# Optimization experiments

Hardware: AMD Instinct MI355X
Metric: run time of the kernel (lower is better)

## Reference

```python
import jax, jax.numpy as jnp
import numpy as np

D_MODEL = 1024
N_HEADS = 16
D_K = 64
D_FF = 4096
B = 8
S = 1024
NEG = -1e32
EPS = 1e-5


def _layer_norm(x, g, b):
    mu = jnp.mean(x, axis=-1, keepdims=True)
    var = jnp.var(x, axis=-1, keepdims=True)
    return (x - mu) * jax.lax.rsqrt(var + EPS) * g + b


def setup_inputs() -> dict:
    key = jax.random.key(0)
    ks = jax.random.split(key, 16)
    sc = 0.02
    inp = {
        'x': jax.random.normal(ks[0], (B, S, D_MODEL), dtype=jnp.float32),
        'Wq': jax.random.normal(ks[1], (D_MODEL, D_MODEL), jnp.float32) * sc,
        'bq': jnp.zeros((D_MODEL,), jnp.float32),
        'Wk': jax.random.normal(ks[2], (D_MODEL, D_MODEL), jnp.float32) * sc,
        'bk': jnp.zeros((D_MODEL,), jnp.float32),
        'Wv': jax.random.normal(ks[3], (D_MODEL, D_MODEL), jnp.float32) * sc,
        'bv': jnp.zeros((D_MODEL,), jnp.float32),
        'Wo': jax.random.normal(ks[4], (D_MODEL, D_MODEL), jnp.float32) * sc,
        'bo': jnp.zeros((D_MODEL,), jnp.float32),
        'W1': jax.random.normal(ks[5], (D_MODEL, D_FF), jnp.float32) * sc,
        'b1': jnp.zeros((D_FF,), jnp.float32),
        'W2': jax.random.normal(ks[6], (D_FF, D_MODEL), jnp.float32) * sc,
        'b2': jnp.zeros((D_MODEL,), jnp.float32),
        'g1': jnp.ones((D_MODEL,), jnp.float32),
        'beta1': jnp.zeros((D_MODEL,), jnp.float32),
        'g3': jnp.ones((D_MODEL,), jnp.float32),
        'beta3': jnp.zeros((D_MODEL,), jnp.float32),
    }
    return inp


def _block(x, Wq, bq, Wk, bk, Wv, bv, Wo, bo, W1, b1, W2, b2, g1, beta1, g3, beta3):
    bs, seqlen, _ = x.shape
    # QKV projections -> [b, h, s, d_k]
    def split_heads(t):
        return t.reshape(bs, seqlen, N_HEADS, D_K).transpose(0, 2, 1, 3)
    q = split_heads(x @ Wq + bq)
    k = split_heads(x @ Wk + bk)
    v = split_heads(x @ Wv + bv)
    # scores [b,h,s,s]
    scores = jnp.einsum('bhqd,bhkd->bhqk', q, k) / jnp.sqrt(jnp.float32(D_K))
    # mask=0 case: src_mask = (triu(ones, k=0) == 0) -> allow strictly lower (j < i)
    i = jnp.arange(seqlen)[:, None]
    j = jnp.arange(seqlen)[None, :]
    allowed = (j < i)  # [s, s]
    scores = jnp.where(allowed[None, None], scores, NEG)
    attn = jax.nn.softmax(scores, axis=-1)
    # zero_pad: zero out the first query row of attention probs
    attn = attn * (i > 0).astype(attn.dtype)[None, None]
    ctx = jnp.einsum('bhqk,bhkd->bhqd', attn, v)  # [b,h,s,d_k]
    concat = ctx.transpose(0, 2, 1, 3).reshape(bs, seqlen, D_MODEL)
    attn_out = concat @ Wo + bo
    # residual + LN (dropout p=0)
    h1 = _layer_norm(x + attn_out, g1, beta1)
    # position-wise FFN
    ffn = jax.nn.relu(h1 @ W1 + b1) @ W2 + b2
    out = _layer_norm(h1 + ffn, g3, beta3)
    return out


def reference(x, Wq, bq, Wk, bk, Wv, bv, Wo, bo, W1, b1, W2, b2, g1, beta1, g3, beta3):
    return _block(x, Wq, bq, Wk, bk, Wv, bv, Wo, bo, W1, b1, W2, b2, g1, beta1, g3, beta3)
```

## Files before the change

### kernel.cpp

```cpp
#include <hip/hip_runtime.h>
#include <hip/hip_bf16.h>

typedef __bf16 bf16x8 __attribute__((ext_vector_type(8)));
typedef __bf16 bf16x4 __attribute__((ext_vector_type(4)));
typedef float f32x4 __attribute__((ext_vector_type(4)));
typedef float f32x16 __attribute__((ext_vector_type(16)));

#define GLOBAL_LOAD_LDS16(gp, lp)                                              \
  __builtin_amdgcn_global_load_lds(                                            \
      (const __attribute__((address_space(1))) void*)(gp),                     \
      (__attribute__((address_space(3))) void*)(lp), 16, 0, 0)

__global__ __launch_bounds__(256) void transpose4_f2b_k(
    const float* __restrict__ s0, const float* __restrict__ s1,
    const float* __restrict__ s2, const float* __restrict__ s3,
    __bf16* __restrict__ dst) {
  __shared__ float tile[32][33];
  const float* srcs[4] = {s0, s1, s2, s3};
  const float* src = srcs[blockIdx.z];
  __bf16* d = dst + ((size_t)blockIdx.z << 20);
  const int bx = blockIdx.x * 32, by = blockIdx.y * 32;
  const int tx = threadIdx.x & 31, ty = threadIdx.x >> 5;
#pragma unroll
  for (int i = 0; i < 32; i += 8)
    tile[ty + i][tx] = src[(size_t)(by + ty + i) * 1024 + bx + tx];
  __syncthreads();
#pragma unroll
  for (int i = 0; i < 32; i += 8)
    d[(size_t)(bx + ty + i) * 1024 + by + tx] = (__bf16)tile[tx][ty + i];
}

__global__ __launch_bounds__(256) void transpose_f2b_k(
    const float* __restrict__ src, __bf16* __restrict__ dst, int R, int C) {
  __shared__ float tile[32][33];
  const int bx = blockIdx.x * 32, by = blockIdx.y * 32;
  const int tx = threadIdx.x & 31, ty = threadIdx.x >> 5;
#pragma unroll
  for (int i = 0; i < 32; i += 8)
    tile[ty + i][tx] = src[(size_t)(by + ty + i) * C + bx + tx];
  __syncthreads();
#pragma unroll
  for (int i = 0; i < 32; i += 8)
    dst[(size_t)(bx + ty + i) * R + by + tx] = (__bf16)tile[tx][ty + i];
}

__global__ __launch_bounds__(256) void transpose_v_k(
    const __bf16* __restrict__ src, __bf16* __restrict__ dst) {
  __shared__ __bf16 tile[32][33];
  const int bh = blockIdx.z;
  const int s0 = blockIdx.x * 32, d0 = blockIdx.y * 32;
  const size_t base = (size_t)bh << 16;
  const int tx = threadIdx.x & 31, ty = threadIdx.x >> 5;
#pragma unroll
  for (int i = 0; i < 32; i += 8)
    tile[ty + i][tx] = src[base + (size_t)(s0 + ty + i) * 64 + d0 + tx];
  __syncthreads();
#pragma unroll
  for (int i = 0; i < 32; i += 8)
    dst[base + (size_t)(d0 + ty + i) * 1024 + s0 + tx] = tile[tx][ty + i];
}

__global__ __launch_bounds__(256) void convert_f2b_k(const float* __restrict__ s,
                                                     __bf16* __restrict__ d) {
  const size_t i = ((size_t)blockIdx.x * 256 + threadIdx.x) * 4;
  const float4 v = *(const float4*)(s + i);
  bf16x4 o;
  o[0] = (__bf16)v.x; o[1] = (__bf16)v.y; o[2] = (__bf16)v.z; o[3] = (__bf16)v.w;
  *(bf16x4*)(d + i) = o;
}

__global__ void concat3_k(const float* a, const float* b, const float* c,
                          float* o) {
  int i = blockIdx.x * 256 + threadIdx.x;
  if (i < 1024) o[i] = a[i];
  else if (i < 2048) o[i] = b[i - 1024];
  else if (i < 3072) o[i] = c[i - 2048];
}

#define STG(P, rowbase, Kld, kbase, DST)                                       \
  do {                                                                         \
    GLOBAL_LOAD_LDS16((P) + (size_t)((rowbase) + wave * 16 + srow) * (Kld) +   \
                          (kbase) + sch8,                                      \
                      (DST) + wave * 1024);                                    \
    GLOBAL_LOAD_LDS16((P) + (size_t)((rowbase) + wave * 16 + 8 + srow) *       \
                              (Kld) + (kbase) + sch8,                          \
                      (DST) + wave * 1024 + 512);                              \
  } while (0)

#define LDA(BUF, HALF)                                                         \
  do {                                                                         \
    const __bf16* pA_ = &As[BUF][HALF][aoff];                                  \
    _Pragma("unroll") for (int f_ = 0; f_ < 4; ++f_) {                         \
      af[f_][0] = *(const bf16x8*)(pA_ + f_ * 1024 + c0);                      \
      af[f_][1] = *(const bf16x8*)(pA_ + f_ * 1024 + (c0 ^ 32));               \
    }                                                                          \
  } while (0)

#define LDB(BUF, CB)                                                           \
  do {                                                                         \
    const __bf16* pB_ = &Bs[BUF][CB][boff];                                    \
    _Pragma("unroll") for (int g_ = 0; g_ < 2; ++g_) {                         \
      bfr[CB][g_][0] = *(const bf16x8*)(pB_ + g_ * 1024 + c0);                 \
      bfr[CB][g_][1] = *(const bf16x8*)(pB_ + g_ * 1024 + (c0 ^ 32));          \
    }                                                                          \
  } while (0)

#define MFMA16(rb, cb)                                                         \
  do {                                                                         \
    _Pragma("unroll") for (int f_ = 0; f_ < 4; ++f_)                           \
        _Pragma("unroll") for (int g_ = 0; g_ < 2; ++g_) {                     \
      acc[rb][f_][cb][g_] = __builtin_amdgcn_mfma_f32_16x16x32_bf16(           \
          af[f_][0], bfr[cb][g_][0], acc[rb][f_][cb][g_], 0, 0, 0);            \
      acc[rb][f_][cb][g_] = __builtin_amdgcn_mfma_f32_16x16x32_bf16(           \
          af[f_][1], bfr[cb][g_][1], acc[rb][f_][cb][g_], 0, 0, 0);            \
    }                                                                          \
  } while (0)

#define PH_MID()                                                               \
  do {                                                                         \
    asm volatile("" ::: "memory");                                             \
    __builtin_amdgcn_s_barrier();                                              \
    asm volatile("s_waitcnt lgkmcnt(0)" ::: "memory");                         \
    __builtin_amdgcn_s_setprio(1);                                             \
  } while (0)

#define PH_END()                                                               \
  do {                                                                         \
    __builtin_amdgcn_s_setprio(0);                                             \
    asm volatile("" ::: "memory");                                             \
    __builtin_amdgcn_s_barrier();                                              \
    asm volatile("" ::: "memory");                                             \
  } while (0)

#define PH_END_VM(NVM)                                                         \
  do {                                                                         \
    __builtin_amdgcn_s_setprio(0);                                             \
    asm volatile("s_waitcnt vmcnt(" #NVM ")" ::: "memory");                    \
    __builtin_amdgcn_s_barrier();                                              \
    asm volatile("" ::: "memory");                                             \
  } while (0)

template <int EPI>
__global__ __launch_bounds__(512, 2) void gemm256(const __bf16* __restrict__ A,
                                                  const __bf16* __restrict__ Bt,
                                                  const float* __restrict__ bias,
                                                  __bf16* __restrict__ C,
                                                  int M, int N, int K) {
  __shared__ __align__(16) __bf16 As[2][2][128 * 64];
  __shared__ __align__(16) __bf16 Bs[2][2][128 * 64];
  const int tid = threadIdx.x;
  const int wave = tid >> 6, lane = tid & 63;
  const int quad = lane >> 4, l15 = lane & 15;
  const int wm = wave >> 2, wn = wave & 3;

  const int nwg = gridDim.x;
  const int cpx = nwg >> 3;
  const int bid = blockIdx.x;
  const int wg = (bid & 7) * cpx + (bid >> 3);
  const int gy = N >> 8;
  const int tm = wg / gy, tn = wg - tm * gy;
  const int m0 = tm << 8, n0 = tn << 8;

  const int srow = lane >> 3;
  const int sch8 = ((lane & 7) ^ srow) * 8;
  const int aoff = (wm * 64 + l15) * 64;
  const int boff = (wn * 32 + l15) * 64;
  const int c0 = (quad ^ (l15 & 7)) * 8;

  bf16x8 af[4][2], bfr[2][2][2];
  f32x4 acc[2][4][2][2] = {};

  const int NJ = K >> 7;

  STG(A, m0, K, 0, &As[0][0][0]);
  STG(Bt, n0, K, 0, &Bs[0][0][0]);
  STG(A, m0 + 128, K, 0, &As[0][1][0]);
  STG(Bt, n0 + 128, K, 0, &Bs[0][1][0]);
  STG(A, m0, K, 64, &As[1][0][0]);
  STG(Bt, n0, K, 64, &Bs[1][0][0]);
  asm volatile("s_waitcnt vmcnt(4)" ::: "memory");
  __builtin_amdgcn_s_barrier();
  asm volatile("" ::: "memory");

  for (int j = 0; j < NJ; ++j) {
    const int t1k = (j << 7) + 64, t2k = (j << 7) + 128, t3k = (j << 7) + 192;
    const bool pf = (j + 1 < NJ);
    LDA(0, 0);
    LDB(0, 0);
    STG(A, m0 + 128, K, t1k, &As[1][1][0]);
    PH_MID();
    MFMA16(0, 0);
    PH_END();
    LDB(0, 1);
    STG(Bt, n0 + 128, K, t1k, &Bs[1][1][0]);
    PH_MID();
    MFMA16(0, 1);
    PH_END();
    LDA(0, 1);
    if (pf) STG(A, m0, K, t2k, &As[0][0][0]);
    PH_MID();
    MFMA16(1, 0);
    PH_END();
    if (pf) STG(Bt, n0, K, t2k, &Bs[0][0][0]);
    PH_MID();
    MFMA16(1, 1);
    if (pf) PH_END_VM(4); else PH_END_VM(0);
    LDA(1, 0);
    LDB(1, 0);
    if (pf) STG(A, m0 + 128, K, t2k, &As[0][1][0]);
    PH_MID();
    MFMA16(0, 0);
    PH_END();
    LDB(1, 1);
    if (pf) STG(Bt, n0 + 128, K, t2k, &Bs[0][1][0]);
    PH_MID();
    MFMA16(0, 1);
    PH_END();
    LDA(1, 1);
    if (pf) STG(A, m0, K, t3k, &As[1][0][0]);
    PH_MID();
    MFMA16(1, 0);
    PH_END();
    if (pf) STG(Bt, n0, K, t3k, &Bs[1][0][0]);
    PH_MID();
    MFMA16(1, 1);
    if (pf) PH_END_VM(4); else PH_END();
  }

  float bvv[2][2];
#pragma unroll
  for (int cb = 0; cb < 2; ++cb)
#pragma unroll
    for (int g = 0; g < 2; ++g)
      bvv[cb][g] = bias[n0 + cb * 128 + wn * 32 + g * 16 + l15];
#pragma unroll
  for (int rb = 0; rb < 2; ++rb)
#pragma unroll
    for (int f = 0; f < 4; ++f)
#pragma unroll
      for (int i = 0; i < 4; ++i) {
        const int row = m0 + rb * 128 + wm * 64 + f * 16 + quad * 4 + i;
#pragma unroll
        for (int cb = 0; cb < 2; ++cb)
#pragma unroll
          for (int g = 0; g < 2; ++g) {
            const int col = n0 + cb * 128 + wn * 32 + g * 16 + l15;
            float v = acc[rb][f][cb][g][i] + bvv[cb][g];
            if (EPI == 1) v = fmaxf(v, 0.0f);
            size_t oidx;
            if (EPI == 2) {
              const int which = col >> 10, wi = col & 1023;
              const int h = wi >> 6, d = wi & 63;
              const int b = row >> 10, s = row & 1023;
              oidx = ((size_t)which << 23) +
                     (((size_t)(b * 16 + h) << 16) + s * 64 + d);
            } else {
              oidx = (size_t)row * N + col;
            }
            C[oidx] = (__bf16)v;
          }
      }
}

__global__ __launch_bounds__(256) void gemm_bt64(const __bf16* __restrict__ A,
                                                 const __bf16* __restrict__ Bt,
                                                 const float* __restrict__ bias,
                                                 __bf16* __restrict__ C,
                                                 int M, int N, int K) {
  __shared__ __align__(16) __bf16 As[128 * 64];
  __shared__ __align__(16) __bf16 Bs[64 * 64];
  const int tid = threadIdx.x;
  const int wave = tid >> 6, lane = tid & 63;
  const int quad = lane >> 4, l15 = lane & 15;
  const int wm = wave >> 1, wn = wave & 1;
  const int m0 = blockIdx.x * 128, n0 = blockIdx.y * 64;
  const int srow = tid >> 3;
  const int sch = tid & 7;

  f32x4 acc[4][2] = {};

  for (int k0 = 0; k0 < K; k0 += 64) {
#pragma unroll
    for (int p = 0; p < 4; ++p) {
      const int row = p * 32 + srow;
      GLOBAL_LOAD_LDS16(A + (size_t)(m0 + row) * K + k0 + ((sch ^ (row & 7)) * 8),
                        As + p * 2048 + wave * 512);
    }
#pragma unroll
    for (int p = 0; p < 2; ++p) {
      const int row = p * 32 + srow;
      GLOBAL_LOAD_LDS16(Bt + (size_t)(n0 + row) * K + k0 + ((sch ^ (row & 7)) * 8),
                        Bs + p * 2048 + wave * 512);
    }
    __syncthreads();
    bf16x8 af[4][2], bfr[2][2];
#pragma unroll
    for (int kk = 0; kk < 2; ++kk) {
#pragma unroll
      for (int mt = 0; mt < 4; ++mt) {
        const int row = wm * 64 + mt * 16 + l15;
        af[mt][kk] =
            *(const bf16x8*)(As + row * 64 + (((kk * 4 + quad) ^ (row & 7)) * 8));
      }
#pragma unroll
      for (int nt = 0; nt < 2; ++nt) {
        const int row = wn * 32 + nt * 16 + l15;
        bfr[nt][kk] =
            *(const bf16x8*)(Bs + row * 64 + (((kk * 4 + quad) ^ (row & 7)) * 8));
      }
    }
#pragma unroll
    for (int kk = 0; kk < 2; ++kk)
#pragma unroll
      for (int mt = 0; mt < 4; ++mt)
#pragma unroll
        for (int nt = 0; nt < 2; ++nt)
          acc[mt][nt] = __builtin_amdgcn_mfma_f32_16x16x32_bf16(
              af[mt][kk], bfr[nt][kk], acc[mt][nt], 0, 0, 0);
    __syncthreads();
  }

  float bv[2];
#pragma unroll
  for (int nt = 0; nt < 2; ++nt) bv[nt] = bias[n0 + wn * 32 + nt * 16 + l15];
#pragma unroll
  for (int mt = 0; mt < 4; ++mt) {
#pragma unroll
    for (int r = 0; r < 4; ++r) {
      const int row = m0 + wm * 64 + mt * 16 + quad * 4 + r;
#pragma unroll
      for (int nt = 0; nt < 2; ++nt) {
        const int col = n0 + wn * 32 + nt * 16 + l15;
        C[(size_t)row * N + col] = (__bf16)(acc[mt][nt][r] + bv[nt]);
      }
    }
  }
}

__global__ __launch_bounds__(256) void attn_kernel(const __bf16* __restrict__ Q,
                                                   const __bf16* __restrict__ Kg,
                                                   const __bf16* __restrict__ Vt,
                                                   __bf16* __restrict__ ctx) {
  const int qp = blockIdx.x;
  const int bh = blockIdx.y;
  const int b = bh >> 4, h = bh & 15;
  const int tid = threadIdx.x, wave = tid >> 6, lane = tid & 63;
  const int quad = lane >> 4, l15 = lane & 15;
  const size_t hoff = (size_t)bh << 16;
  const __bf16* Qh = Q + hoff;
  const __bf16* Kh = Kg + hoff;
  const __bf16* Vh = Vt + hoff;

  __shared__ __align__(16) __bf16 Ks[64 * 64];
  __shared__ __align__(16) __bf16 Vs[64 * 64];
  __shared__ __align__(16) __bf16 Ps[4][32 * 72];
  __shared__ float lL[128];

  const int skey = wave * 8 + (lane >> 3);
  const int sgr = lane & 7;

#pragma unroll
  for (int pass = 0; pass < 2; ++pass) {
    const int qt = pass ? (7 - qp) : qp;
    const int qb = qt * 128;

    bf16x8 qf[2][2];
#pragma unroll
    for (int g = 0; g < 2; ++g) {
      const int qrow = qb + wave * 32 + g * 16 + l15;
      bf16x8 t0 = *(const bf16x8*)(Qh + (size_t)qrow * 64 + quad * 8);
      bf16x8 t1 = *(const bf16x8*)(Qh + (size_t)qrow * 64 + 32 + quad * 8);
#pragma unroll
      for (int e = 0; e < 8; ++e) {
        qf[g][0][e] = (__bf16)((float)t0[e] * 0.125f);
        qf[g][1][e] = (__bf16)((float)t1[e] * 0.125f);
      }
    }

    f32x4 oacc[4][2] = {};
    float lrun[2][4] = {};

    const int ktmax = 2 * qt + 1;
    for (int kt = 0; kt <= ktmax; ++kt) {
      __syncthreads();
#pragma unroll
      for (int j = 0; j < 2; ++j) {
        const int row = skey + 32 * j;
        GLOBAL_LOAD_LDS16(
            Kh + (size_t)(kt * 64 + row) * 64 + ((sgr ^ (row & 7)) * 8),
            Ks + j * 2048 + wave * 512);
        GLOBAL_LOAD_LDS16(
            Vh + (size_t)row * 1024 + kt * 64 + ((sgr ^ (row & 7)) * 8),
            Vs + j * 2048 + wave * 512);
      }
      __syncthreads();

      f32x4 sacc[2][4] = {};
#pragma unroll
      for (int nt = 0; nt < 4; ++nt) {
        const int key = nt * 16 + l15, sw = key & 7;
        bf16x8 kf0 = *(const bf16x8*)(Ks + key * 64 + ((quad ^ sw) * 8));
        bf16x8 kf1 = *(const bf16x8*)(Ks + key * 64 + (((quad + 4) ^ sw) * 8));
#pragma unroll
        for (int g = 0; g < 2; ++g) {
          sacc[g][nt] = __builtin_amdgcn_mfma_f32_16x16x32_bf16(
              qf[g][0], kf0, sacc[g][nt], 0, 0, 0);
          sacc[g][nt] = __builtin_amdgcn_mfma_f32_16x16x32_bf16(
              qf[g][1], kf1, sacc[g][nt], 0, 0, 0);
        }
      }

      const bool tilemask = (kt >= 2 * qt);
#pragma unroll
      for (int g = 0; g < 2; ++g)
#pragma unroll
        for (int nt = 0; nt < 4; ++nt) {
          const int key = kt * 64 + nt * 16 + l15;
#pragma unroll
          for (int r = 0; r < 4; ++r) {
            float p = __expf(fminf(sacc[g][nt][r], 60.0f));
            if (tilemask && key >= qb + wave * 32 + g * 16 + quad * 4 + r)
              p = 0.0f;
            sacc[g][nt][r] = p;
            lrun[g][r] += p;
          }
        }

#pragma unroll
      for (int g = 0; g < 2; ++g)
#pragma unroll
        for (int nt = 0; nt < 4; ++nt)
#pragma unroll
          for (int r = 0; r < 4; ++r)
            Ps[wave][(g * 16 + quad * 4 + r) * 72 + nt * 16 + l15] =
                (__bf16)sacc[g][nt][r];

#pragma unroll
      for (int kc = 0; kc < 2; ++kc) {
        bf16x8 pf[2];
#pragma unroll
        for (int g = 0; g < 2; ++g)
          pf[g] = *(const bf16x8*)(&Ps[wave][(g * 16 + l15) * 72 + kc * 32 +
                                             quad * 8]);
#pragma unroll
        for (int mdt = 0; mdt < 4; ++mdt) {
          const int d = mdt * 16 + l15, sw = d & 7;
          bf16x8 vf =
              *(const bf16x8*)(Vs + d * 64 + (((kc * 4 + quad) ^ sw) * 8));
#pragma unroll
          for (int g = 0; g < 2; ++g)
            oacc[mdt][g] = __builtin_amdgcn_mfma_f32_16x16x32_bf16(
                vf, pf[g], oacc[mdt][g], 0, 0, 0);
        }
      }
    }

#pragma unroll
    for (int g = 0; g < 2; ++g)
#pragma unroll
      for (int r = 0; r < 4; ++r) {
        float s = lrun[g][r];
#pragma unroll
        for (int d = 1; d < 16; d <<= 1) s += __shfl_xor(s, d);
        if (l15 == 0) lL[wave * 32 + g * 16 + quad * 4 + r] = s;
      }
    float linv[2];
#pragma unroll
    for (int g = 0; g < 2; ++g) {
      const float l = lL[wave * 32 + g * 16 + l15];
      linv[g] = (qb + wave * 32 + g * 16 + l15 == 0) ? 0.0f : (1.0f / l);
    }
    __bf16* Ot = Ps[wave];
#pragma unroll
    for (int mdt = 0; mdt < 4; ++mdt)
#pragma unroll
      for (int g = 0; g < 2; ++g)
#pragma unroll
        for (int r = 0; r < 4; ++r)
          Ot[(g * 16 + l15) * 72 + mdt * 16 + quad * 4 + r] =
              (__bf16)(oacc[mdt][g][r] * linv[g]);
#pragma unroll
    for (int rr = 0; rr < 2; ++rr)
#pragma unroll
      for (int j = 0; j < 2; ++j) {
        const int row = rr * 16 + (lane >> 2), chk = (lane & 3) + 4 * j;
        bf16x8 ov = *(const bf16x8*)(Ot + row * 72 + chk * 8);
        const size_t oi = ((size_t)(b * 1024 + qb + wave * 32 + row)) * 1024 +
                          h * 64 + chk * 8;
        *(bf16x8*)(ctx + oi) = ov;
      }
  }
}

template <typename TX, typename TY, typename TO>
__global__ __launch_bounds__(256) void add_ln_kernel(const TX* __restrict__ x,
                                                     const TY* __restrict__ y,
                                                     const float* __restrict__ g,
                                                     const float* __restrict__ be,
                                                     TO* __restrict__ out) {
  const int row = blockIdx.x;
  const size_t base = (size_t)row * 1024;
  const int t = threadIdx.x;
  float xv[4], yv[4];
  if constexpr (sizeof(TX) == 4) {
    const float4 a = *(const float4*)(x + base + t * 4);
    xv[0] = a.x; xv[1] = a.y; xv[2] = a.z; xv[3] = a.w;
  } else {
    const bf16x4 a = *(const bf16x4*)(x + base + t * 4);
#pragma unroll
    for (int i = 0; i < 4; ++i) xv[i] = (float)a[i];
  }
  if constexpr (sizeof(TY) == 4) {
    const float4 a = *(const float4*)(y + base + t * 4);
    yv[0] = a.x; yv[1] = a.y; yv[2] = a.z; yv[3] = a.w;
  } else {
    const bf16x4 a = *(const bf16x4*)(y + base + t * 4);
#pragma unroll
    for (int i = 0; i < 4; ++i) yv[i] = (float)a[i];
  }
  float v[4], s = 0.0f, s2 = 0.0f;
#pragma unroll
  for (int i = 0; i < 4; ++i) {
    v[i] = xv[i] + yv[i];
    s += v[i];
    s2 += v[i] * v[i];
  }
#pragma unroll
  for (int m = 1; m < 64; m <<= 1) {
    s += __shfl_xor(s, m);
    s2 += __shfl_xor(s2, m);
  }
  __shared__ float ss[4], ss2[4];
  const int w = t >> 6;
  if ((t & 63) == 0) { ss[w] = s; ss2[w] = s2; }
  __syncthreads();
  s = ss[0] + ss[1] + ss[2] + ss[3];
  s2 = ss2[0] + ss2[1] + ss2[2] + ss2[3];
  const float mu = s * (1.0f / 1024.0f);
  const float var = s2 * (1.0f / 1024.0f) - mu * mu;
  const float rstd = rsqrtf(var + 1e-5f);
#pragma unroll
  for (int i = 0; i < 4; ++i) {
    const float o = (v[i] - mu) * rstd * g[t * 4 + i] + be[t * 4 + i];
    out[base + t * 4 + i] = (TO)o;
  }
}

extern "C" void kernel_launch(void* const* d_in, const int* in_sizes, int n_in,
                              void* d_out, int out_size, void* d_ws,
                              size_t ws_size, hipStream_t stream) {
  (void)in_sizes; (void)n_in; (void)out_size; (void)ws_size;
  const float* x   = (const float*)d_in[0];
  const float* Wq  = (const float*)d_in[1];
  const float* bq  = (const float*)d_in[2];
  const float* Wk  = (const float*)d_in[3];
  const float* bk  = (const float*)d_in[4];
  const float* Wv  = (const float*)d_in[5];
  const float* bv  = (const float*)d_in[6];
  const float* Wo  = (const float*)d_in[7];
  const float* bo  = (const float*)d_in[8];
  const float* W1  = (const float*)d_in[9];
  const float* b1  = (const float*)d_in[10];
  const float* W2  = (const float*)d_in[11];
  const float* b2  = (const float*)d_in[12];
  const float* g1  = (const float*)d_in[13];
  const float* be1 = (const float*)d_in[14];
  const float* g3  = (const float*)d_in[15];
  const float* be3 = (const float*)d_in[16];

  char* ws = (char*)d_ws;
  __bf16* Qb    = (__bf16*)(ws + 0);
  __bf16* Kb    = (__bf16*)(ws + (16u << 20));
  __bf16* Vb    = (__bf16*)(ws + (32u << 20));
  __bf16* ctx   = (__bf16*)(ws + (48u << 20));
  __bf16* mid   = (__bf16*)(ws + 0);
  __bf16* aout  = (__bf16*)(ws + (64u << 20));
  __bf16* h1    = aout;
  __bf16* xb    = (__bf16*)(ws + (80u << 20));
  __bf16* Vtb   = (__bf16*)(ws + (80u << 20));
  __bf16* fout  = (__bf16*)(ws + (80u << 20));
  __bf16* WqkvT = (__bf16*)(ws + (96u << 20));
  __bf16* WoT   = (__bf16*)(ws + (96u << 20) + 3 * (1u << 21));
  __bf16* W1T   = (__bf16*)(ws + (104u << 20));
  __bf16* W2T   = (__bf16*)(ws + (112u << 20));
  float*  bqkv  = (float*)(ws + (120u << 20));
  float*  outp  = (float*)d_out;

  const dim3 blk(256);
  const dim3 blk512(512);
  convert_f2b_k<<<dim3(8192), blk, 0, stream>>>(x, xb);
  transpose4_f2b_k<<<dim3(32, 32, 4), blk, 0, stream>>>(Wq, Wk, Wv, Wo, WqkvT);
  transpose_f2b_k<<<dim3(128, 32), blk, 0, stream>>>(W1, W1T, 1024, 4096);
  transpose_f2b_k<<<dim3(32, 128), blk, 0, stream>>>(W2, W2T, 4096, 1024);
  concat3_k<<<dim3(12), blk, 0, stream>>>(bq, bk, bv, bqkv);

  gemm256<2><<<dim3(32 * 12), blk512, 0, stream>>>(xb, WqkvT, bqkv, Qb,
                                                   8192, 3072, 1024);
  transpose_v_k<<<dim3(32, 2, 128), blk, 0, stream>>>(Vb, Vtb);
  attn_kernel<<<dim3(4, 128), blk, 0, stream>>>(Qb, Kb, Vtb, ctx);
  gemm_bt64<<<dim3(64, 16), blk, 0, stream>>>(ctx, WoT, bo, aout, 8192, 1024, 1024);
  add_ln_kernel<float, __bf16, __bf16><<<dim3(8192), blk, 0, stream>>>(
      x, aout, g1, be1, h1);
  gemm256<1><<<dim3(32 * 16), blk512, 0, stream>>>(h1, W1T, b1, mid,
                                                   8192, 4096, 1024);
  gemm_bt64<<<dim3(64, 16), blk, 0, stream>>>(mid, W2T, b2, fout, 8192, 1024, 4096);
  add_ln_kernel<__bf16, __bf16, float><<<dim3(8192), blk, 0, stream>>>(
      h1, fout, g3, be3, outp);
}
```

Baseline: 510.0 us.

## Replace simple 128x64 GEMM with pipelined 256x128 double-buffered GEMM for N=1024

Replaces the single-stage 128x64 tile GEMM used for the Wo and W2 projections with a new 256x128 tile, 512-thread kernel. It uses double-buffered LDS with async global-to-LDS loads, phased barriers with setprio, and a grouped (XCD-aware) block ordering, modelled on the existing gemm256. The aim is to hide global-load latency and raise MFMA utilisation compared with the old kernel, which synchronised on every k-step. The trade-off is only 256 workgroups for N=1024, which may underfill the 256 CUs, plus higher LDS and register use per block. The PH_* macros are also moved earlier in the file so both kernels can use them.

```diff
diff --git a/kernel.cpp b/kernel.cpp
--- a/kernel.cpp
+++ b/kernel.cpp
@@ -87,6 +87,30 @@
                       (DST) + wave * 1024 + 512);                              \
   } while (0)
 
+#define PH_MID()                                                               \
+  do {                                                                         \
+    asm volatile("" ::: "memory");                                             \
+    __builtin_amdgcn_s_barrier();                                              \
+    asm volatile("s_waitcnt lgkmcnt(0)" ::: "memory");                         \
+    __builtin_amdgcn_s_setprio(1);                                             \
+  } while (0)
+
+#define PH_END()                                                               \
+  do {                                                                         \
+    __builtin_amdgcn_s_setprio(0);                                             \
+    asm volatile("" ::: "memory");                                             \
+    __builtin_amdgcn_s_barrier();                                              \
+    asm volatile("" ::: "memory");                                             \
+  } while (0)
+
+#define PH_END_VM(NVM)                                                         \
+  do {                                                                         \
+    __builtin_amdgcn_s_setprio(0);                                             \
+    asm volatile("s_waitcnt vmcnt(" #NVM ")" ::: "memory");                    \
+    __builtin_amdgcn_s_barrier();                                              \
+    asm volatile("" ::: "memory");                                             \
+  } while (0)
+
 #define LDA(BUF, HALF)                                                         \
   do {                                                                         \
     const __bf16* pA_ = &As[BUF][HALF][aoff];                                  \
@@ -114,30 +138,6 @@
       acc[rb][f_][cb][g_] = __builtin_amdgcn_mfma_f32_16x16x32_bf16(           \
           af[f_][1], bfr[cb][g_][1], acc[rb][f_][cb][g_], 0, 0, 0);            \
     }                                                                          \
-  } while (0)
-
-#define PH_MID()                                                               \
-  do {                                                                         \
-    asm volatile("" ::: "memory");                                             \
-    __builtin_amdgcn_s_barrier();                                              \
-    asm volatile("s_waitcnt lgkmcnt(0)" ::: "memory");                         \
-    __builtin_amdgcn_s_setprio(1);                                             \
-  } while (0)
-
-#define PH_END()                                                               \
-  do {                                                                         \
-    __builtin_amdgcn_s_setprio(0);                                             \
-    asm volatile("" ::: "memory");                                             \
-    __builtin_amdgcn_s_barrier();                                              \
-    asm volatile("" ::: "memory");                                             \
-  } while (0)
-
-#define PH_END_VM(NVM)                                                         \
-  do {                                                                         \
-    __builtin_amdgcn_s_setprio(0);                                             \
-    asm volatile("s_waitcnt vmcnt(" #NVM ")" ::: "memory");                    \
-    __builtin_amdgcn_s_barrier();                                              \
-    asm volatile("" ::: "memory");                                             \
   } while (0)
 
 template <int EPI>
@@ -262,79 +262,124 @@
       }
 }
 
-__global__ __launch_bounds__(256) void gemm_bt64(const __bf16* __restrict__ A,
-                                                 const __bf16* __restrict__ Bt,
-                                                 const float* __restrict__ bias,
-                                                 __bf16* __restrict__ C,
-                                                 int M, int N, int K) {
-  __shared__ __align__(16) __bf16 As[128 * 64];
-  __shared__ __align__(16) __bf16 Bs[64 * 64];
+#define LDAN(BUF, HALF)                                                        \
+  do {                                                                         \
+    const __bf16* pA_ = &As[BUF][HALF][aoff];                                  \
+    _Pragma("unroll") for (int f_ = 0; f_ < 4; ++f_) {                         \
+      af[f_][0] = *(const bf16x8*)(pA_ + f_ * 1024 + c0);                      \
+      af[f_][1] = *(const bf16x8*)(pA_ + f_ * 1024 + (c0 ^ 32));               \
+    }                                                                          \
+  } while (0)
+
+#define LDBN(BUF)                                                              \
+  do {                                                                         \
+    const __bf16* pB_ = &Bs[BUF][boff];                                        \
+    _Pragma("unroll") for (int g_ = 0; g_ < 2; ++g_) {                         \
+      bfr[g_][0] = *(const bf16x8*)(pB_ + g_ * 1024 + c0);                     \
+      bfr[g_][1] = *(const bf16x8*)(pB_ + g_ * 1024 + (c0 ^ 32));              \
+    }                                                                          \
+  } while (0)
+
+#define MFMAN(rb)                                                              \
+  do {                                                                         \
+    _Pragma("unroll") for (int f_ = 0; f_ < 4; ++f_)                           \
+        _Pragma("unroll") for (int g_ = 0; g_ < 2; ++g_) {                     \
+      acc[rb][f_][g_] = __builtin_amdgcn_mfma_f32_16x16x32_bf16(               \
+          af[f_][0], bfr[g_][0], acc[rb][f_][g_], 0, 0, 0);                    \
+      acc[rb][f_][g_] = __builtin_amdgcn_mfma_f32_16x16x32_bf16(               \
+          af[f_][1], bfr[g_][1], acc[rb][f_][g_], 0, 0, 0);                    \
+    }                                                                          \
+  } while (0)
+
+template <int EPI>
+__global__ __launch_bounds__(512, 2) void gemm256n(const __bf16* __restrict__ A,
+                                                   const __bf16* __restrict__ Bt,
+                                                   const float* __restrict__ bias,
+                                                   __bf16* __restrict__ C,
+                                                   int M, int N, int K) {
+  __shared__ __align__(16) __bf16 As[2][2][128 * 64];
+  __shared__ __align__(16) __bf16 Bs[2][128 * 64];
   const int tid = threadIdx.x;
   const int wave = tid >> 6, lane = tid & 63;
   const int quad = lane >> 4, l15 = lane & 15;
-  const int wm = wave >> 1, wn = wave & 1;
-  const int m0 = blockIdx.x * 128, n0 = blockIdx.y * 64;
-  const int srow = tid >> 3;
-  const int sch = tid & 7;
-
-  f32x4 acc[4][2] = {};
-
-  for (int k0 = 0; k0 < K; k0 += 64) {
-#pragma unroll
-    for (int p = 0; p < 4; ++p) {
-      const int row = p * 32 + srow;
-      GLOBAL_LOAD_LDS16(A + (size_t)(m0 + row) * K + k0 + ((sch ^ (row & 7)) * 8),
-                        As + p * 2048 + wave * 512);
+  const int wm = wave >> 2, wn = wave & 3;
+
+  const int nwg = gridDim.x;
+  const int cpx = nwg >> 3;
+  const int bid = blockIdx.x;
+  const int wg = (bid & 7) * cpx + (bid >> 3);
+  const int gy = N >> 7;
+  const int tm = wg / gy, tn = wg - tm * gy;
+  const int m0 = tm << 8, n0 = tn << 7;
+
+  const int srow = lane >> 3;
+  const int sch8 = ((lane & 7) ^ srow) * 8;
+  const int aoff = (wm * 64 + l15) * 64;
+  const int boff = (wn * 32 + l15) * 64;
+  const int c0 = (quad ^ (l15 & 7)) * 8;
+
+  bf16x8 af[4][2], bfr[2][2];
+  f32x4 acc[2][4][2] = {};
+
+  const int NJ = K >> 7;
+
+  STG(A, m0, K, 0, &As[0][0][0]);
+  STG(Bt, n0, K, 0, &Bs[0][0]);
+  STG(A, m0 + 128, K, 0, &As[0][1][0]);
+  STG(A, m0, K, 64, &As[1][0][0]);
+  asm volatile("s_waitcnt vmcnt(2)" ::: "memory");
+  __builtin_amdgcn_s_barrier();
+  asm volatile("" ::: "memory");
+
+  for (int j = 0; j < NJ; ++j) {
+    const int t1k = (j << 7) + 64, t2k = (j << 7) + 128, t3k = (j << 7) + 192;
+    const bool pf = (j + 1 < NJ);
+    LDAN(0, 0);
+    LDBN(0);
+    STG(Bt, n0, K, t1k, &Bs[1][0]);
+    STG(A, m0 + 128, K, t1k, &As[1][1][0]);
+    PH_MID();
+    MFMAN(0);
+    PH_END();
+    LDAN(0, 1);
+    if (pf) STG(A, m0, K, t2k, &As[0][0][0]);
+    PH_MID();
+    MFMAN(1);
+    if (pf) PH_END_VM(2); else PH_END_VM(0);
+    LDAN(1, 0);
+    LDBN(1);
+    if (pf) {
+      STG(A, m0 + 128, K, t2k, &As[0][1][0]);
+      STG(Bt, n0, K, t2k, &Bs[0][0]);
     }
-#pragma unroll
-    for (int p = 0; p < 2; ++p) {
-      const int row = p * 32 + srow;
-      GLOBAL_LOAD_LDS16(Bt + (size_t)(n0 + row) * K + k0 + ((sch ^ (row & 7)) * 8),
-                        Bs + p * 2048 + wave * 512);
-    }
-    __syncthreads();
-    bf16x8 af[4][2], bfr[2][2];
-#pragma unroll
-    for (int kk = 0; kk < 2; ++kk) {
-#pragma unroll
-      for (int mt = 0; mt < 4; ++mt) {
-        const int row = wm * 64 + mt * 16 + l15;
-        af[mt][kk] =
-            *(const bf16x8*)(As + row * 64 + (((kk * 4 + quad) ^ (row & 7)) * 8));
-      }
-#pragma unroll
-      for (int nt = 0; nt < 2; ++nt) {
-        const int row = wn * 32 + nt * 16 + l15;
-        bfr[nt][kk] =
-            *(const bf16x8*)(Bs + row * 64 + (((kk * 4 + quad) ^ (row & 7)) * 8));
-      }
-    }
-#pragma unroll
-    for (int kk = 0; kk < 2; ++kk)
-#pragma unroll
-      for (int mt = 0; mt < 4; ++mt)
-#pragma unroll
-        for (int nt = 0; nt < 2; ++nt)
-          acc[mt][nt] = __builtin_amdgcn_mfma_f32_16x16x32_bf16(
-              af[mt][kk], bfr[nt][kk], acc[mt][nt], 0, 0, 0);
-    __syncthreads();
-  }
-
-  float bv[2];
-#pragma unroll
-  for (int nt = 0; nt < 2; ++nt) bv[nt] = bias[n0 + wn * 32 + nt * 16 + l15];
-#pragma unroll
-  for (int mt = 0; mt < 4; ++mt) {
-#pragma unroll
-    for (int r = 0; r < 4; ++r) {
-      const int row = m0 + wm * 64 + mt * 16 + quad * 4 + r;
-#pragma unroll
-      for (int nt = 0; nt < 2; ++nt) {
-        const int col = n0 + wn * 32 + nt * 16 + l15;
-        C[(size_t)row * N + col] = (__bf16)(acc[mt][nt][r] + bv[nt]);
-      }
-    }
-  }
+    PH_MID();
+    MFMAN(0);
+    PH_END();
+    LDAN(1, 1);
+    if (pf) STG(A, m0, K, t3k, &As[1][0][0]);
+    PH_MID();
+    MFMAN(1);
+    if (pf) PH_END_VM(2); else PH_END();
+  }
+
+  float bvv[2];
+#pragma unroll
+  for (int g = 0; g < 2; ++g) bvv[g] = bias[n0 + wn * 32 + g * 16 + l15];
+#pragma unroll
+  for (int rb = 0; rb < 2; ++rb)
+#pragma unroll
+    for (int f = 0; f < 4; ++f)
+#pragma unroll
+      for (int i = 0; i < 4; ++i) {
+        const int row = m0 + rb * 128 + wm * 64 + f * 16 + quad * 4 + i;
+#pragma unroll
+        for (int g = 0; g < 2; ++g) {
+          const int col = n0 + wn * 32 + g * 16 + l15;
+          float v = acc[rb][f][g][i] + bvv[g];
+          if (EPI == 1) v = fmaxf(v, 0.0f);
+          C[(size_t)row * N + col] = (__bf16)v;
+        }
+      }
 }
 
 __global__ __launch_bounds__(256) void attn_kernel(const __bf16* __restrict__ Q,
@@ -598,12 +643,14 @@
                                                    8192, 3072, 1024);
   transpose_v_k<<<dim3(32, 2, 128), blk, 0, stream>>>(Vb, Vtb);
   attn_kernel<<<dim3(4, 128), blk, 0, stream>>>(Qb, Kb, Vtb, ctx);
-  gemm_bt64<<<dim3(64, 16), blk, 0, stream>>>(ctx, WoT, bo, aout, 8192, 1024, 1024);
+  gemm256n<0><<<dim3(32 * 8), blk512, 0, stream>>>(ctx, WoT, bo, aout,
+                                                   8192, 1024, 1024);
   add_ln_kernel<float, __bf16, __bf16><<<dim3(8192), blk, 0, stream>>>(
       x, aout, g1, be1, h1);
   gemm256<1><<<dim3(32 * 16), blk512, 0, stream>>>(h1, W1T, b1, mid,
                                                    8192, 4096, 1024);
-  gemm_bt64<<<dim3(64, 16), blk, 0, stream>>>(mid, W2T, b2, fout, 8192, 1024, 4096);
+  gemm256n<0><<<dim3(32 * 8), blk512, 0, stream>>>(mid, W2T, b2, fout,
+                                                   8192, 1024, 4096);
   add_ln_kernel<__bf16, __bf16, float><<<dim3(8192), blk, 0, stream>>>(
       h1, fout, g3, be3, outp);
 }
```

After: 501.8 us. About the same (-1.6%).
